# Kernel optimization log

Hardware: AMD Instinct MI355X
Metric: run time of the kernel (lower is better)

The kernel has to match this reference:

```python
import jax, jax.numpy as jnp
import numpy as np

B, C, H, NP, M = 32, 768, 12, 196, 64
D = C // H
GRID = 14  # sqrt(196)
NG = 1 + NP  # cls + patches = 197
EPS = 1e-5


def _ln(x, w, b):
    mu = x.mean(-1, keepdims=True)
    var = ((x - mu) ** 2).mean(-1, keepdims=True)
    return (x - mu) * jax.lax.rsqrt(var + EPS) * w + b


def setup_inputs() -> dict:
    key = jax.random.key(0)
    ks = jax.random.split(key, 14)
    std = 0.02
    return {
        "x": jax.random.normal(ks[0], (B, NG + M, C), dtype=jnp.float32),
        "ps": jax.random.uniform(ks[1], (B, M, 2), dtype=jnp.float32) * 224.0,
        "ns": jax.random.randint(ks[2], (B,), 1, M + 1, dtype=jnp.int32),
        "norm1_w": jnp.ones((C,), jnp.float32),
        "norm1_b": jnp.zeros((C,), jnp.float32),
        "qkv_w": jax.random.normal(ks[3], (3 * C, C), jnp.float32) * std,
        "proj_w": jax.random.normal(ks[4], (C, C), jnp.float32) * std,
        "proj_b": jnp.zeros((C,), jnp.float32),
        "norm2_w": jnp.ones((C,), jnp.float32),
        "norm2_b": jnp.zeros((C,), jnp.float32),
        "fc1_w": jax.random.normal(ks[5], (4 * C, C), jnp.float32) * std,
        "fc1_b": jnp.zeros((4 * C,), jnp.float32),
        "fc2_w": jax.random.normal(ks[6], (C, 4 * C), jnp.float32) * std,
        "fc2_b": jnp.zeros((C,), jnp.float32),
    }


def reference(x, ps, ns, norm1_w, norm1_b, qkv_w, proj_w, proj_b,
              norm2_w, norm2_b, fc1_w, fc1_b, fc2_w, fc2_b):
    Bn, Nt, Cd = x.shape  # Nt = 1 + 196 + M
    scale = D ** -0.5

    h = _ln(x, norm1_w, norm1_b)
    qkv = (h @ qkv_w.T).reshape(Bn, Nt, 3, H, D).transpose(2, 0, 3, 1, 4)  # [3,B,H,Nt,D]
    q, k, v = qkv[0], qkv[1], qkv[2]

    # ---- global attention over cls + patch tokens (first 197) ----
    attn = jnp.einsum('bhnd,bhmd->bhnm', q[:, :, :NG], k[:, :, :NG]) * scale
    attn = jax.nn.softmax(attn, axis=-1)
    xg = jnp.einsum('bhnm,bhmd->bhnd', attn, v[:, :, :NG])
    xg = xg.transpose(0, 2, 1, 3).reshape(Bn, NG, Cd)  # [B,197,C]

    # ---- keypoint bilinear-gather attention (get_single_filter_matrix) ----
    pos = ps / 16.0  # [B,M,2]; pos[...,1] -> row (dim 4), pos[...,0] -> col (dim 5)
    c0 = jnp.clip(jnp.floor(pos[..., 0]), 0, GRID - 1).astype(jnp.int32)
    c1 = jnp.clip(jnp.ceil(pos[..., 0]), 0, GRID - 1).astype(jnp.int32)
    r0 = jnp.clip(jnp.floor(pos[..., 1]), 0, GRID - 1).astype(jnp.int32)
    r1 = jnp.clip(jnp.ceil(pos[..., 1]), 0, GRID - 1).astype(jnp.int32)
    # neighbor order: top_left, top_right, bottom_left, bottom_right
    rows = jnp.stack([r0, r1, r0, r1], axis=-1)  # [B,M,4]
    cols = jnp.stack([c0, c0, c1, c1], axis=-1)
    flat = rows * GRID + cols  # [B,M,4] flat index into 196 patch tokens

    kp = k[:, :, 1:NG]  # [B,H,196,D]
    vp = v[:, :, 1:NG]
    idx = jnp.broadcast_to(flat.reshape(Bn, 1, M * 4, 1), (Bn, H, M * 4, D))
    knb = jnp.take_along_axis(kp, idx, axis=2).reshape(Bn, H, M, 4, D)
    vnb = jnp.take_along_axis(vp, idx, axis=2).reshape(Bn, H, M, 4, D)

    qk = q[:, :, NG:]  # keypoint queries [B,H,M,D]
    a = jnp.einsum('bhmd,bhmjd->bhmj', qk, knb)  # no scale, per original
    a = jax.nn.softmax(a, axis=-1)
    kout = jnp.einsum('bhmj,bhmjd->bhmd', a, vnb)
    kout = kout.transpose(0, 2, 1, 3).reshape(Bn, M, Cd)

    y = jnp.concatenate([xg, kout], axis=1) @ proj_w.T + proj_b
    x = x + y

    h2 = _ln(x, norm2_w, norm2_b)
    h2 = jax.nn.gelu(h2 @ fc1_w.T + fc1_b, approximate=False)
    x = x + (h2 @ fc2_w.T + fc2_b)
    return x
```

## Files before the change

kernel.cpp:

```cpp
#include <hip/hip_runtime.h>

typedef unsigned short u16;
typedef unsigned int u32;
typedef u16 u16x8 __attribute__((ext_vector_type(8)));
typedef u16 u16x4 __attribute__((ext_vector_type(4)));
typedef float f32x4 __attribute__((ext_vector_type(4)));
typedef __bf16 bf16x8 __attribute__((ext_vector_type(8)));

#define NHEAD 12
#define NT 261
#define NGL 197
#define CDIM 768
#define KT 14
#define PS_STRIDE 232
#define VT_STRIDE 232

__device__ __forceinline__ float bf2f(u16 u) {
    u32 x = ((u32)u) << 16;
    float f;
    __builtin_memcpy(&f, &x, 4);
    return f;
}
__device__ __forceinline__ u16 f2bf(float f) {
    u32 x;
    __builtin_memcpy(&x, &f, 4);
    x = (x + 0x7fffu + ((x >> 16) & 1u)) >> 16;
    return (u16)x;
}

#define GLD_LDS16(g, l) \
    __builtin_amdgcn_global_load_lds((const __attribute__((address_space(1))) void*)(g), \
                                     (__attribute__((address_space(3))) void*)(l), 16, 0, 0)
#define WAITV(n) asm volatile("s_waitcnt vmcnt(" #n ")" ::: "memory")
#define BARM() asm volatile("s_barrier" ::: "memory")

__global__ __launch_bounds__(256) void convk(const float* __restrict__ in, u16* __restrict__ out, int n4) {
    int i = blockIdx.x * 256 + threadIdx.x;
    if (i >= n4) return;
    float4 v = ((const float4*)in)[i];
    u16x4 o;
    o[0] = f2bf(v.x); o[1] = f2bf(v.y); o[2] = f2bf(v.z); o[3] = f2bf(v.w);
    ((u16x4*)out)[i] = o;
}

__global__ __launch_bounds__(256) void ln_k(const float* __restrict__ in, const float* __restrict__ w,
                                            const float* __restrict__ bia, u16* __restrict__ out) {
    int row = blockIdx.x;
    int tid = threadIdx.x;
    const float* r = in + (size_t)row * CDIM;
    float v0 = r[tid], v1 = r[tid + 256], v2 = r[tid + 512];
    float s = v0 + v1 + v2;
    float ss = v0 * v0 + v1 * v1 + v2 * v2;
#pragma unroll
    for (int off = 32; off; off >>= 1) {
        s += __shfl_xor(s, off);
        ss += __shfl_xor(ss, off);
    }
    __shared__ float ls[4], lss[4];
    int wv = tid >> 6;
    if ((tid & 63) == 0) { ls[wv] = s; lss[wv] = ss; }
    __syncthreads();
    s = ls[0] + ls[1] + ls[2] + ls[3];
    ss = lss[0] + lss[1] + lss[2] + lss[3];
    float mu = s * (1.f / 768.f);
    float var = ss * (1.f / 768.f) - mu * mu;
    float inv = rsqrtf(var + 1e-5f);
    u16* o = out + (size_t)row * CDIM;
    o[tid]       = f2bf((v0 - mu) * inv * w[tid]       + bia[tid]);
    o[tid + 256] = f2bf((v1 - mu) * inv * w[tid + 256] + bia[tid + 256]);
    o[tid + 512] = f2bf((v2 - mu) * inv * w[tid + 512] + bia[tid + 512]);
}

template <int EPI>
__global__ __launch_bounds__(256, 2) void gemm3(const u16* __restrict__ A, const u16* __restrict__ Bw,
                                                int M, int N, int K, int nbn,
                                                const float* __restrict__ bias,
                                                const float* __restrict__ resid, void* __restrict__ outp) {
    __shared__ __align__(16) u16 sm[4][8192];
    const int tid = threadIdx.x;
    const int nwg = gridDim.x;
    const int q = nwg >> 3, r = nwg & 7;
    const int xcd = blockIdx.x & 7, within = blockIdx.x >> 3;
    const int id2 = (xcd < r ? xcd * (q + 1) : r * (q + 1) + (xcd - r) * q) + within;
    const int bm = id2 / nbn, bn = id2 % nbn;
    const int lane = tid & 63, wv = tid >> 6;
    const int wr = wv >> 1, wc = wv & 1;
    const int l15 = lane & 15, lg = lane >> 4;
    const int arow0 = bm * 128, brow0 = bn * 128;
    const int nt = K >> 5;

    const int srow = tid >> 2;
    const int sslot = tid & 3;
    const int sk0 = (sslot ^ ((srow >> 1) & 3)) * 8;
    int arA0 = arow0 + srow;        if (arA0 >= M) arA0 = M - 1;
    int arA1 = arow0 + srow + 64;   if (arA1 >= M) arA1 = M - 1;
    const u16* gA0 = A + (size_t)arA0 * K + sk0;
    const u16* gA1 = A + (size_t)arA1 * K + sk0;
    const u16* gB0 = Bw + (size_t)(brow0 + srow) * K + sk0;
    const u16* gB1 = Bw + (size_t)(brow0 + srow + 64) * K + sk0;
    const int lo0 = tid * 8, lo1 = 2048 + tid * 8;

    auto STAGE = [&](int tt) {
        u16* b = sm[tt & 3];
        const size_t ko = (size_t)tt * 32;
        GLD_LDS16(gA0 + ko, b + lo0);
        GLD_LDS16(gA1 + ko, b + lo1);
        GLD_LDS16(gB0 + ko, b + 4096 + lo0);
        GLD_LDS16(gB1 + ko, b + 4096 + lo1);
    };

    f32x4 acc[4][4] = {};
    const int xorv = (lg ^ ((l15 >> 1) & 3)) << 3;

    STAGE(0); STAGE(1); STAGE(2);
    for (int t = 0; t < nt; ++t) {
        if (t + 2 < nt) { WAITV(8); } else if (t + 1 < nt) { WAITV(4); } else { WAITV(0); }
        BARM();
        if (t + 3 < nt) STAGE(t + 3);
        const u16* bufp = sm[t & 3];
        bf16x8 af[4], bfr[4];
#pragma unroll
        for (int mi = 0; mi < 4; ++mi)
            af[mi] = *(const bf16x8*)(bufp + (wr * 64 + mi * 16 + l15) * 32 + xorv);
#pragma unroll
        for (int ni = 0; ni < 4; ++ni)
            bfr[ni] = *(const bf16x8*)(bufp + 4096 + (wc * 64 + ni * 16 + l15) * 32 + xorv);
#pragma unroll
        for (int mi = 0; mi < 4; ++mi)
#pragma unroll
            for (int ni = 0; ni < 4; ++ni)
                acc[mi][ni] = __builtin_amdgcn_mfma_f32_16x16x32_bf16(af[mi], bfr[ni], acc[mi][ni], 0, 0, 0);
    }

#pragma unroll
    for (int mi = 0; mi < 4; ++mi) {
        int row0 = arow0 + wr * 64 + mi * 16 + lg * 4;
#pragma unroll
        for (int ni = 0; ni < 4; ++ni) {
            int col = brow0 + wc * 64 + ni * 16 + l15;
            float bb = (EPI == 0) ? 0.f : bias[col];
#pragma unroll
            for (int rr = 0; rr < 4; ++rr) {
                int row = row0 + rr;
                if (row < M) {
                    float v = acc[mi][ni][rr] + bb;
                    if (EPI == 2) {
                        float z = v + 0.044715f * v * v * v;
                        v = v / (1.f + __expf(-1.5957691216f * z));
                    }
                    if (EPI == 1) {
                        v += resid[(size_t)row * N + col];
                        ((float*)outp)[(size_t)row * N + col] = v;
                    } else {
                        ((u16*)outp)[(size_t)row * N + col] = f2bf(v);
                    }
                }
            }
        }
    }
}

__global__ __launch_bounds__(256) void attn_global_mfma(const u16* __restrict__ qkv, u16* __restrict__ Z) {
    __shared__ __align__(16) u16 lds0[4 * 16 * PS_STRIDE];
    __shared__ __align__(16) u16 Vt[64 * VT_STRIDE];
    const int tid = threadIdx.x;
    const int blk = blockIdx.x;
    const int qt = blk & 3;
    const int bh = blk >> 2;
    const int h = bh % NHEAD, b = bh / NHEAD;
    const int lane = tid & 63, wv = tid >> 6;
    const int l15 = lane & 15, lg = lane >> 4;
    const u16* base = qkv + (size_t)b * NT * 2304;

    for (int c = tid; c < 224 * 8; c += 256) {
        int row = c >> 3, ch = c & 7;
        u16x8 v = {};
        if (row < NGL) v = *(const u16x8*)(base + (size_t)row * 2304 + 768 + h * 64 + ch * 8);
        int byte = row * 128 + ((ch * 16) ^ ((row & 7) << 4));
        *(u16x8*)((char*)lds0 + byte) = v;
    }
    for (int c = tid; c < 112 * 8; c += 256) {
        int mp = c >> 3, dch = c & 7;
        int m0 = mp * 2;
        u16x8 a0 = {}, a1 = {};
        if (m0 < NGL)     a0 = *(const u16x8*)(base + (size_t)m0 * 2304 + 1536 + h * 64 + dch * 8);
        if (m0 + 1 < NGL) a1 = *(const u16x8*)(base + (size_t)(m0 + 1) * 2304 + 1536 + h * 64 + dch * 8);
#pragma unroll
        for (int j = 0; j < 8; ++j) {
            u32 pk = (u32)a0[j] | ((u32)a1[j] << 16);
            *(u32*)((char*)Vt + (size_t)(dch * 8 + j) * (VT_STRIDE * 2) + m0 * 2) = pk;
        }
    }
    const int q0 = qt * 64 + wv * 16;
    int qrow = q0 + l15; if (qrow > NGL - 1) qrow = NGL - 1;
    bf16x8 aq0 = *(const bf16x8*)(base + (size_t)qrow * 2304 + h * 64 + lg * 8);
    bf16x8 aq1 = *(const bf16x8*)(base + (size_t)qrow * 2304 + h * 64 + 32 + lg * 8);
    __syncthreads();

    f32x4 s[KT];
    const int sw = (l15 & 7) << 4;
#pragma unroll
    for (int t = 0; t < KT; ++t) {
        const char* krow = (const char*)lds0 + (t * 16 + l15) * 128;
        bf16x8 bk0 = *(const bf16x8*)(krow + ((lg * 16) ^ sw));
        bf16x8 bk1 = *(const bf16x8*)(krow + ((64 + lg * 16) ^ sw));
        f32x4 acc = {};
        acc = __builtin_amdgcn_mfma_f32_16x16x32_bf16(aq0, bk0, acc, 0, 0, 0);
        acc = __builtin_amdgcn_mfma_f32_16x16x32_bf16(aq1, bk1, acc, 0, 0, 0);
        s[t] = acc * 0.125f;
    }
    float mx[4] = {-1e30f, -1e30f, -1e30f, -1e30f};
#pragma unroll
    for (int t = 0; t < KT; ++t)
#pragma unroll
        for (int r = 0; r < 4; ++r) mx[r] = fmaxf(mx[r], s[t][r]);
#pragma unroll
    for (int off = 1; off < 16; off <<= 1)
#pragma unroll
        for (int r = 0; r < 4; ++r) mx[r] = fmaxf(mx[r], __shfl_xor(mx[r], off));
    float sum[4] = {};
#pragma unroll
    for (int t = 0; t < KT; ++t) {
        bool valid = (t * 16 + l15) < NGL;
#pragma unroll
        for (int r = 0; r < 4; ++r) {
            float e = valid ? __expf(s[t][r] - mx[r]) : 0.f;
            s[t][r] = e;
            sum[r] += e;
        }
    }
#pragma unroll
    for (int off = 1; off < 16; off <<= 1)
#pragma unroll
        for (int r = 0; r < 4; ++r) sum[r] += __shfl_xor(sum[r], off);
    float inv[4];
#pragma unroll
    for (int r = 0; r < 4; ++r) inv[r] = 1.f / sum[r];

    __syncthreads();
    u16* Pw = lds0 + wv * 16 * PS_STRIDE;
#pragma unroll
    for (int t = 0; t < KT; ++t)
#pragma unroll
        for (int r = 0; r < 4; ++r)
            Pw[(4 * lg + r) * PS_STRIDE + t * 16 + l15] = f2bf(s[t][r] * inv[r]);

    f32x4 o[4] = {};
#pragma unroll
    for (int ks = 0; ks < 7; ++ks) {
        bf16x8 pa = *(const bf16x8*)(Pw + l15 * PS_STRIDE + ks * 32 + lg * 8);
#pragma unroll
        for (int dt = 0; dt < 4; ++dt) {
            bf16x8 bv = *(const bf16x8*)((const char*)Vt + (size_t)(dt * 16 + l15) * (VT_STRIDE * 2) + ks * 64 + lg * 16);
            o[dt] = __builtin_amdgcn_mfma_f32_16x16x32_bf16(pa, bv, o[dt], 0, 0, 0);
        }
    }
#pragma unroll
    for (int dt = 0; dt < 4; ++dt)
#pragma unroll
        for (int r = 0; r < 4; ++r) {
            int q = q0 + 4 * lg + r;
            if (q < NGL) Z[((size_t)b * NT + q) * CDIM + h * 64 + dt * 16 + l15] = f2bf(o[dt][r]);
        }
}

__global__ __launch_bounds__(64) void attn_neigh(const u16* __restrict__ qkv, const float* __restrict__ ps,
                                                 u16* __restrict__ Z) {
    int blk = blockIdx.x;
    int b = blk >> 6, m = blk & 63;
    int lane = threadIdx.x;
    float px = ps[((size_t)b * 64 + m) * 2 + 0] * (1.f / 16.f);
    float py = ps[((size_t)b * 64 + m) * 2 + 1] * (1.f / 16.f);
    int c0 = min(max((int)floorf(px), 0), 13);
    int c1 = min(max((int)ceilf(px), 0), 13);
    int r0 = min(max((int)floorf(py), 0), 13);
    int r1 = min(max((int)ceilf(py), 0), 13);
    int tok[4];
    tok[0] = 1 + r0 * 14 + c0;
    tok[1] = 1 + r1 * 14 + c0;
    tok[2] = 1 + r0 * 14 + c1;
    tok[3] = 1 + r1 * 14 + c1;
    const size_t rowq = ((size_t)b * NT + NGL + m) * 2304;
#pragma unroll 1
    for (int h = 0; h < NHEAD; ++h) {
        float qv = bf2f(qkv[rowq + h * 64 + lane]);
        float a[4];
#pragma unroll
        for (int j = 0; j < 4; ++j) {
            float p = qv * bf2f(qkv[((size_t)b * NT + tok[j]) * 2304 + 768 + h * 64 + lane]);
#pragma unroll
            for (int off = 32; off; off >>= 1) p += __shfl_xor(p, off);
            a[j] = p;
        }
        float mx = fmaxf(fmaxf(a[0], a[1]), fmaxf(a[2], a[3]));
        float e0 = expf(a[0] - mx), e1 = expf(a[1] - mx), e2 = expf(a[2] - mx), e3 = expf(a[3] - mx);
        float inv = 1.f / (e0 + e1 + e2 + e3);
        float v0 = bf2f(qkv[((size_t)b * NT + tok[0]) * 2304 + 1536 + h * 64 + lane]);
        float v1 = bf2f(qkv[((size_t)b * NT + tok[1]) * 2304 + 1536 + h * 64 + lane]);
        float v2 = bf2f(qkv[((size_t)b * NT + tok[2]) * 2304 + 1536 + h * 64 + lane]);
        float v3 = bf2f(qkv[((size_t)b * NT + tok[3]) * 2304 + 1536 + h * 64 + lane]);
        float o = (e0 * v0 + e1 * v1 + e2 * v2 + e3 * v3) * inv;
        Z[((size_t)b * NT + NGL + m) * CDIM + h * 64 + lane] = f2bf(o);
    }
}

extern "C" void kernel_launch(void* const* d_in, const int* in_sizes, int n_in,
                              void* d_out, int out_size, void* d_ws, size_t ws_size,
                              hipStream_t stream) {
    const float* x      = (const float*)d_in[0];
    const float* ps     = (const float*)d_in[1];
    const float* n1w    = (const float*)d_in[3];
    const float* n1b    = (const float*)d_in[4];
    const float* qkv_w  = (const float*)d_in[5];
    const float* proj_w = (const float*)d_in[6];
    const float* proj_b = (const float*)d_in[7];
    const float* n2w    = (const float*)d_in[8];
    const float* n2b    = (const float*)d_in[9];
    const float* fc1_w  = (const float*)d_in[10];
    const float* fc1_b  = (const float*)d_in[11];
    const float* fc2_w  = (const float*)d_in[12];
    const float* fc2_b  = (const float*)d_in[13];

    char* ws = (char*)d_ws;
    const int M = 32 * NT;
    u16* hbuf  = (u16*)ws;
    u16* qkvb  = (u16*)(ws + 12828672);
    u16* Zb    = (u16*)(ws + 12828672 + 38486016);
    u16* Gb    = (u16*)(ws + 12828672);
    float* x1  = (float*)(ws + 64143360);
    u16* wq    = (u16*)(ws + 89800704);
    u16* wp    = wq + 2304 * 768;
    u16* w1    = wp + 768 * 768;
    u16* w2    = w1 + 3072 * 768;

    convk<<<(2304 * 768 / 4 + 255) / 256, 256, 0, stream>>>(qkv_w, wq, 2304 * 768 / 4);
    convk<<<(768 * 768 / 4 + 255) / 256, 256, 0, stream>>>(proj_w, wp, 768 * 768 / 4);
    convk<<<(3072 * 768 / 4 + 255) / 256, 256, 0, stream>>>(fc1_w, w1, 3072 * 768 / 4);
    convk<<<(768 * 3072 / 4 + 255) / 256, 256, 0, stream>>>(fc2_w, w2, 768 * 3072 / 4);

    ln_k<<<M, 256, 0, stream>>>(x, n1w, n1b, hbuf);
    gemm3<0><<<66 * 18, 256, 0, stream>>>(hbuf, wq, M, 2304, 768, 18, nullptr, nullptr, qkvb);
    attn_global_mfma<<<32 * NHEAD * 4, 256, 0, stream>>>(qkvb, Zb);
    attn_neigh<<<32 * 64, 64, 0, stream>>>(qkvb, ps, Zb);
    gemm3<1><<<66 * 6, 256, 0, stream>>>(Zb, wp, M, 768, 768, 6, proj_b, x, x1);
    ln_k<<<M, 256, 0, stream>>>(x1, n2w, n2b, hbuf);
    gemm3<2><<<66 * 24, 256, 0, stream>>>(hbuf, w1, M, 3072, 768, 24, fc1_b, nullptr, Gb);
    gemm3<1><<<66 * 6, 256, 0, stream>>>(Gb, w2, M, 768, 3072, 6, fc2_b, x1, (float*)d_out);
}
```

Measured before the change: 322.6 us.

## Store GEMM operands in MFMA fragment layout and load directly without LDS

The weights, layernorm outputs, attention output and GELU output are written in a pre-tiled MFMA fragment layout, so each GEMM wave reads its bf16x8 fragments straight from global memory and the LDS staging, barriers and async copies go away. The four weight conversions are merged with the first layernorm into one launch, layernorm now uses one wave per row, and neighbour attention is folded into the global attention kernel as extra blocks. This removes launch overhead and LDS traffic, but drops the explicit multi-stage prefetch pipeline and data reuse through shared memory. The GEMM now depends on L1/L2 caching and on latency being hidden by occupancy.

After: 343.5 us. 1.06x slower.

```diff
diff --git a/kernel.cpp b/kernel.cpp
--- a/kernel.cpp
+++ b/kernel.cpp
@@ -28,55 +28,94 @@
     return (u16)x;
 }
 
-#define GLD_LDS16(g, l) \
-    __builtin_amdgcn_global_load_lds((const __attribute__((address_space(1))) void*)(g), \
-                                     (__attribute__((address_space(3))) void*)(l), 16, 0, 0)
-#define WAITV(n) asm volatile("s_waitcnt vmcnt(" #n ")" ::: "memory")
-#define BARM() asm volatile("s_barrier" ::: "memory")
-
-__global__ __launch_bounds__(256) void convk(const float* __restrict__ in, u16* __restrict__ out, int n4) {
-    int i = blockIdx.x * 256 + threadIdx.x;
-    if (i >= n4) return;
-    float4 v = ((const float4*)in)[i];
-    u16x4 o;
-    o[0] = f2bf(v.x); o[1] = f2bf(v.y); o[2] = f2bf(v.z); o[3] = f2bf(v.w);
-    ((u16x4*)out)[i] = o;
-}
-
-__global__ __launch_bounds__(256) void ln_k(const float* __restrict__ in, const float* __restrict__ w,
-                                            const float* __restrict__ bia, u16* __restrict__ out) {
-    int row = blockIdx.x;
-    int tid = threadIdx.x;
-    const float* r = in + (size_t)row * CDIM;
-    float v0 = r[tid], v1 = r[tid + 256], v2 = r[tid + 512];
-    float s = v0 + v1 + v2;
-    float ss = v0 * v0 + v1 * v1 + v2 * v2;
+__device__ __forceinline__ size_t fragAddr(int row, int col, int Kd) {
+    return ((size_t)((row >> 4) * (Kd >> 5) + (col >> 5))) * 512 +
+           ((((col >> 3) & 3) * 16 + (row & 15)) * 8 + (col & 7));
+}
+
+struct CvArgs {
+    const float* in[4];
+    u16* out[4];
+    int n8[4];
+    int K[4];
+};
+
+__device__ __forceinline__ void ln_row(const float* __restrict__ in, const float* __restrict__ w,
+                                       const float* __restrict__ bia, u16* __restrict__ out,
+                                       int row, int lane) {
+    const float4* r = (const float4*)(in + (size_t)row * CDIM);
+    float4 a = r[lane], b4 = r[lane + 64], c4 = r[lane + 128];
+    float s  = a.x + a.y + a.z + a.w + b4.x + b4.y + b4.z + b4.w + c4.x + c4.y + c4.z + c4.w;
+    float ss = a.x*a.x + a.y*a.y + a.z*a.z + a.w*a.w
+             + b4.x*b4.x + b4.y*b4.y + b4.z*b4.z + b4.w*b4.w
+             + c4.x*c4.x + c4.y*c4.y + c4.z*c4.z + c4.w*c4.w;
 #pragma unroll
     for (int off = 32; off; off >>= 1) {
-        s += __shfl_xor(s, off);
+        s  += __shfl_xor(s, off);
         ss += __shfl_xor(ss, off);
     }
-    __shared__ float ls[4], lss[4];
-    int wv = tid >> 6;
-    if ((tid & 63) == 0) { ls[wv] = s; lss[wv] = ss; }
-    __syncthreads();
-    s = ls[0] + ls[1] + ls[2] + ls[3];
-    ss = lss[0] + lss[1] + lss[2] + lss[3];
     float mu = s * (1.f / 768.f);
     float var = ss * (1.f / 768.f) - mu * mu;
     float inv = rsqrtf(var + 1e-5f);
-    u16* o = out + (size_t)row * CDIM;
-    o[tid]       = f2bf((v0 - mu) * inv * w[tid]       + bia[tid]);
-    o[tid + 256] = f2bf((v1 - mu) * inv * w[tid + 256] + bia[tid + 256]);
-    o[tid + 512] = f2bf((v2 - mu) * inv * w[tid + 512] + bia[tid + 512]);
+    const float4* wp = (const float4*)w;
+    const float4* bp = (const float4*)bia;
+#pragma unroll
+    for (int t = 0; t < 3; ++t) {
+        float4 v = (t == 0) ? a : (t == 1) ? b4 : c4;
+        float4 ww = wp[lane + t * 64], bb = bp[lane + t * 64];
+        u16x4 ov;
+        ov[0] = f2bf((v.x - mu) * inv * ww.x + bb.x);
+        ov[1] = f2bf((v.y - mu) * inv * ww.y + bb.y);
+        ov[2] = f2bf((v.z - mu) * inv * ww.z + bb.z);
+        ov[3] = f2bf((v.w - mu) * inv * ww.w + bb.w);
+        int col = t * 256 + lane * 4;
+        *(u16x4*)(out + fragAddr(row, col, 768)) = ov;
+    }
+}
+
+__global__ __launch_bounds__(256) void pre_k(const float* __restrict__ x, const float* __restrict__ w,
+                                             const float* __restrict__ bia, u16* __restrict__ out,
+                                             int nrows, CvArgs cv) {
+    if (blockIdx.y == 0) {
+        int i = blockIdx.x * 256 + threadIdx.x;
+        int s0 = cv.n8[0], s1 = s0 + cv.n8[1], s2 = s1 + cv.n8[2], s3 = s2 + cv.n8[3];
+        int seg, base;
+        if (i < s0)      { seg = 0; base = 0; }
+        else if (i < s1) { seg = 1; base = s0; }
+        else if (i < s2) { seg = 2; base = s1; }
+        else if (i < s3) { seg = 3; base = s2; }
+        else return;
+        int j = i - base;
+        int Kd = cv.K[seg];
+        int kd8 = Kd >> 3;
+        int n = j / kd8;
+        int k8 = j - n * kd8;
+        const float* src = cv.in[seg] + (size_t)n * Kd + k8 * 8;
+        float4 v0 = *(const float4*)src;
+        float4 v1 = *(const float4*)(src + 4);
+        u16x8 ov;
+        ov[0] = f2bf(v0.x); ov[1] = f2bf(v0.y); ov[2] = f2bf(v0.z); ov[3] = f2bf(v0.w);
+        ov[4] = f2bf(v1.x); ov[5] = f2bf(v1.y); ov[6] = f2bf(v1.z); ov[7] = f2bf(v1.w);
+        *(u16x8*)(cv.out[seg] + fragAddr(n, k8 * 8, Kd)) = ov;
+    } else {
+        int lane = threadIdx.x & 63, wv = threadIdx.x >> 6;
+        int row = blockIdx.x * 4 + wv;
+        if (row < nrows) ln_row(x, w, bia, out, row, lane);
+    }
+}
+
+__global__ __launch_bounds__(256) void ln_w(const float* __restrict__ in, const float* __restrict__ w,
+                                            const float* __restrict__ bia, u16* __restrict__ out, int nrows) {
+    int lane = threadIdx.x & 63, wv = threadIdx.x >> 6;
+    int row = blockIdx.x * 4 + wv;
+    if (row < nrows) ln_row(in, w, bia, out, row, lane);
 }
 
 template <int EPI>
-__global__ __launch_bounds__(256, 2) void gemm3(const u16* __restrict__ A, const u16* __restrict__ Bw,
-                                                int M, int N, int K, int nbn,
-                                                const float* __restrict__ bias,
-                                                const float* __restrict__ resid, void* __restrict__ outp) {
-    __shared__ __align__(16) u16 sm[4][8192];
+__global__ __launch_bounds__(256) void gemm10(const u16* __restrict__ Ap, const u16* __restrict__ Bp,
+                                              int M, int N, int K, int nbn,
+                                              const float* __restrict__ bias,
+                                              const float* __restrict__ resid, void* __restrict__ outp) {
     const int tid = threadIdx.x;
     const int nwg = gridDim.x;
     const int q = nwg >> 3, r = nwg & 7;
@@ -86,73 +125,62 @@
     const int lane = tid & 63, wv = tid >> 6;
     const int wr = wv >> 1, wc = wv & 1;
     const int l15 = lane & 15, lg = lane >> 4;
-    const int arow0 = bm * 128, brow0 = bn * 128;
-    const int nt = K >> 5;
-
-    const int srow = tid >> 2;
-    const int sslot = tid & 3;
-    const int sk0 = (sslot ^ ((srow >> 1) & 3)) * 8;
-    int arA0 = arow0 + srow;        if (arA0 >= M) arA0 = M - 1;
-    int arA1 = arow0 + srow + 64;   if (arA1 >= M) arA1 = M - 1;
-    const u16* gA0 = A + (size_t)arA0 * K + sk0;
-    const u16* gA1 = A + (size_t)arA1 * K + sk0;
-    const u16* gB0 = Bw + (size_t)(brow0 + srow) * K + sk0;
-    const u16* gB1 = Bw + (size_t)(brow0 + srow + 64) * K + sk0;
-    const int lo0 = tid * 8, lo1 = 2048 + tid * 8;
-
-    auto STAGE = [&](int tt) {
-        u16* b = sm[tt & 3];
-        const size_t ko = (size_t)tt * 32;
-        GLD_LDS16(gA0 + ko, b + lo0);
-        GLD_LDS16(gA1 + ko, b + lo1);
-        GLD_LDS16(gB0 + ko, b + 4096 + lo0);
-        GLD_LDS16(gB1 + ko, b + 4096 + lo1);
-    };
+    const int nt = K >> 6;
+    const int kch = K >> 5;
+    const int mtmax = (M - 1) >> 4;
+
+    const u16* aB[4];
+    const u16* bB[4];
+#pragma unroll
+    for (int i = 0; i < 4; ++i) {
+        int mt = bm * 8 + wr * 4 + i;
+        if (mt > mtmax) mt = mtmax;
+        aB[i] = Ap + (size_t)mt * kch * 512 + lane * 8;
+        bB[i] = Bp + (size_t)(bn * 8 + wc * 4 + i) * kch * 512 + lane * 8;
+    }
 
     f32x4 acc[4][4] = {};
-    const int xorv = (lg ^ ((l15 >> 1) & 3)) << 3;
-
-    STAGE(0); STAGE(1); STAGE(2);
+#pragma unroll 1
     for (int t = 0; t < nt; ++t) {
-        if (t + 2 < nt) { WAITV(8); } else if (t + 1 < nt) { WAITV(4); } else { WAITV(0); }
-        BARM();
-        if (t + 3 < nt) STAGE(t + 3);
-        const u16* bufp = sm[t & 3];
-        bf16x8 af[4], bfr[4];
+        bf16x8 af[4][2], bf[4][2];
+#pragma unroll
+        for (int i = 0; i < 4; ++i) {
+            af[i][0] = *(const bf16x8*)(aB[i] + (size_t)(2 * t) * 512);
+            af[i][1] = *(const bf16x8*)(aB[i] + (size_t)(2 * t + 1) * 512);
+            bf[i][0] = *(const bf16x8*)(bB[i] + (size_t)(2 * t) * 512);
+            bf[i][1] = *(const bf16x8*)(bB[i] + (size_t)(2 * t + 1) * 512);
+        }
 #pragma unroll
         for (int mi = 0; mi < 4; ++mi)
-            af[mi] = *(const bf16x8*)(bufp + (wr * 64 + mi * 16 + l15) * 32 + xorv);
-#pragma unroll
-        for (int ni = 0; ni < 4; ++ni)
-            bfr[ni] = *(const bf16x8*)(bufp + 4096 + (wc * 64 + ni * 16 + l15) * 32 + xorv);
-#pragma unroll
-        for (int mi = 0; mi < 4; ++mi)
-#pragma unroll
-            for (int ni = 0; ni < 4; ++ni)
-                acc[mi][ni] = __builtin_amdgcn_mfma_f32_16x16x32_bf16(af[mi], bfr[ni], acc[mi][ni], 0, 0, 0);
-    }
-
+#pragma unroll
+            for (int ni = 0; ni < 4; ++ni) {
+                acc[mi][ni] = __builtin_amdgcn_mfma_f32_16x16x32_bf16(af[mi][0], bf[ni][0], acc[mi][ni], 0, 0, 0);
+                acc[mi][ni] = __builtin_amdgcn_mfma_f32_16x16x32_bf16(af[mi][1], bf[ni][1], acc[mi][ni], 0, 0, 0);
+            }
+    }
+
+    const int arow0 = bm * 128, bcol0 = bn * 128;
 #pragma unroll
     for (int mi = 0; mi < 4; ++mi) {
         int row0 = arow0 + wr * 64 + mi * 16 + lg * 4;
 #pragma unroll
         for (int ni = 0; ni < 4; ++ni) {
-            int col = brow0 + wc * 64 + ni * 16 + l15;
+            int col = bcol0 + wc * 64 + ni * 16 + l15;
             float bb = (EPI == 0) ? 0.f : bias[col];
 #pragma unroll
             for (int rr = 0; rr < 4; ++rr) {
                 int row = row0 + rr;
                 if (row < M) {
                     float v = acc[mi][ni][rr] + bb;
-                    if (EPI == 2) {
-                        float z = v + 0.044715f * v * v * v;
-                        v = v / (1.f + __expf(-1.5957691216f * z));
-                    }
-                    if (EPI == 1) {
+                    if (EPI == 0) {
+                        ((u16*)outp)[(size_t)row * N + col] = f2bf(v);
+                    } else if (EPI == 1) {
                         v += resid[(size_t)row * N + col];
                         ((float*)outp)[(size_t)row * N + col] = v;
                     } else {
-                        ((u16*)outp)[(size_t)row * N + col] = f2bf(v);
+                        float z = v + 0.044715f * v * v * v;
+                        v = v / (1.f + __expf(-1.5957691216f * z));
+                        ((u16*)outp)[fragAddr(row, col, N)] = f2bf(v);
                     }
                 }
             }
@@ -160,15 +188,58 @@
     }
 }
 
-__global__ __launch_bounds__(256) void attn_global_mfma(const u16* __restrict__ qkv, u16* __restrict__ Z) {
+__global__ __launch_bounds__(256) void attn_fused(const u16* __restrict__ qkv, const float* __restrict__ ps,
+                                                  u16* __restrict__ Z) {
     __shared__ __align__(16) u16 lds0[4 * 16 * PS_STRIDE];
     __shared__ __align__(16) u16 Vt[64 * VT_STRIDE];
     const int tid = threadIdx.x;
+    const int lane = tid & 63, wv = tid >> 6;
+
+    if (blockIdx.x >= 1536) {
+        int idx = blockIdx.x - 1536;
+        int b = idx >> 4;
+        int m = (idx & 15) * 4 + wv;
+        float px = ps[((size_t)b * 64 + m) * 2 + 0] * (1.f / 16.f);
+        float py = ps[((size_t)b * 64 + m) * 2 + 1] * (1.f / 16.f);
+        int c0 = min(max((int)floorf(px), 0), 13);
+        int c1 = min(max((int)ceilf(px), 0), 13);
+        int r0 = min(max((int)floorf(py), 0), 13);
+        int r1 = min(max((int)ceilf(py), 0), 13);
+        int tok[4];
+        tok[0] = 1 + r0 * 14 + c0;
+        tok[1] = 1 + r1 * 14 + c0;
+        tok[2] = 1 + r0 * 14 + c1;
+        tok[3] = 1 + r1 * 14 + c1;
+        const size_t rowq = ((size_t)b * NT + NGL + m) * 2304;
+        const int zrow = b * NT + NGL + m;
+#pragma unroll 1
+        for (int h = 0; h < NHEAD; ++h) {
+            float qv = bf2f(qkv[rowq + h * 64 + lane]);
+            float a[4];
+#pragma unroll
+            for (int j = 0; j < 4; ++j) {
+                float p = qv * bf2f(qkv[((size_t)b * NT + tok[j]) * 2304 + 768 + h * 64 + lane]);
+#pragma unroll
+                for (int off = 32; off; off >>= 1) p += __shfl_xor(p, off);
+                a[j] = p;
+            }
+            float mx = fmaxf(fmaxf(a[0], a[1]), fmaxf(a[2], a[3]));
+            float e0 = expf(a[0] - mx), e1 = expf(a[1] - mx), e2 = expf(a[2] - mx), e3 = expf(a[3] - mx);
+            float inv = 1.f / (e0 + e1 + e2 + e3);
+            float v0 = bf2f(qkv[((size_t)b * NT + tok[0]) * 2304 + 1536 + h * 64 + lane]);
+            float v1 = bf2f(qkv[((size_t)b * NT + tok[1]) * 2304 + 1536 + h * 64 + lane]);
+            float v2 = bf2f(qkv[((size_t)b * NT + tok[2]) * 2304 + 1536 + h * 64 + lane]);
+            float v3 = bf2f(qkv[((size_t)b * NT + tok[3]) * 2304 + 1536 + h * 64 + lane]);
+            float o = (e0 * v0 + e1 * v1 + e2 * v2 + e3 * v3) * inv;
+            Z[fragAddr(zrow, h * 64 + lane, 768)] = f2bf(o);
+        }
+        return;
+    }
+
     const int blk = blockIdx.x;
     const int qt = blk & 3;
     const int bh = blk >> 2;
     const int h = bh % NHEAD, b = bh / NHEAD;
-    const int lane = tid & 63, wv = tid >> 6;
     const int l15 = lane & 15, lg = lane >> 4;
     const u16* base = qkv + (size_t)b * NT * 2304;
 
@@ -259,49 +330,9 @@
     for (int dt = 0; dt < 4; ++dt)
 #pragma unroll
         for (int r = 0; r < 4; ++r) {
-            int q = q0 + 4 * lg + r;
-            if (q < NGL) Z[((size_t)b * NT + q) * CDIM + h * 64 + dt * 16 + l15] = f2bf(o[dt][r]);
-        }
-}
-
-__global__ __launch_bounds__(64) void attn_neigh(const u16* __restrict__ qkv, const float* __restrict__ ps,
-                                                 u16* __restrict__ Z) {
-    int blk = blockIdx.x;
-    int b = blk >> 6, m = blk & 63;
-    int lane = threadIdx.x;
-    float px = ps[((size_t)b * 64 + m) * 2 + 0] * (1.f / 16.f);
-    float py = ps[((size_t)b * 64 + m) * 2 + 1] * (1.f / 16.f);
-    int c0 = min(max((int)floorf(px), 0), 13);
-    int c1 = min(max((int)ceilf(px), 0), 13);
-    int r0 = min(max((int)floorf(py), 0), 13);
-    int r1 = min(max((int)ceilf(py), 0), 13);
-    int tok[4];
-    tok[0] = 1 + r0 * 14 + c0;
-    tok[1] = 1 + r1 * 14 + c0;
-    tok[2] = 1 + r0 * 14 + c1;
-    tok[3] = 1 + r1 * 14 + c1;
-    const size_t rowq = ((size_t)b * NT + NGL + m) * 2304;
-#pragma unroll 1
-    for (int h = 0; h < NHEAD; ++h) {
-        float qv = bf2f(qkv[rowq + h * 64 + lane]);
-        float a[4];
-#pragma unroll
-        for (int j = 0; j < 4; ++j) {
-            float p = qv * bf2f(qkv[((size_t)b * NT + tok[j]) * 2304 + 768 + h * 64 + lane]);
-#pragma unroll
-            for (int off = 32; off; off >>= 1) p += __shfl_xor(p, off);
-            a[j] = p;
-        }
-        float mx = fmaxf(fmaxf(a[0], a[1]), fmaxf(a[2], a[3]));
-        float e0 = expf(a[0] - mx), e1 = expf(a[1] - mx), e2 = expf(a[2] - mx), e3 = expf(a[3] - mx);
-        float inv = 1.f / (e0 + e1 + e2 + e3);
-        float v0 = bf2f(qkv[((size_t)b * NT + tok[0]) * 2304 + 1536 + h * 64 + lane]);
-        float v1 = bf2f(qkv[((size_t)b * NT + tok[1]) * 2304 + 1536 + h * 64 + lane]);
-        float v2 = bf2f(qkv[((size_t)b * NT + tok[2]) * 2304 + 1536 + h * 64 + lane]);
-        float v3 = bf2f(qkv[((size_t)b * NT + tok[3]) * 2304 + 1536 + h * 64 + lane]);
-        float o = (e0 * v0 + e1 * v1 + e2 * v2 + e3 * v3) * inv;
-        Z[((size_t)b * NT + NGL + m) * CDIM + h * 64 + lane] = f2bf(o);
-    }
+            int qq = q0 + 4 * lg + r;
+            if (qq < NGL) Z[fragAddr(b * NT + qq, h * 64 + dt * 16 + l15, 768)] = f2bf(o[dt][r]);
+        }
 }
 
 extern "C" void kernel_launch(void* const* d_in, const int* in_sizes, int n_in,
@@ -333,17 +364,17 @@
     u16* w1    = wp + 768 * 768;
     u16* w2    = w1 + 3072 * 768;
 
-    convk<<<(2304 * 768 / 4 + 255) / 256, 256, 0, stream>>>(qkv_w, wq, 2304 * 768 / 4);
-    convk<<<(768 * 768 / 4 + 255) / 256, 256, 0, stream>>>(proj_w, wp, 768 * 768 / 4);
-    convk<<<(3072 * 768 / 4 + 255) / 256, 256, 0, stream>>>(fc1_w, w1, 3072 * 768 / 4);
-    convk<<<(768 * 3072 / 4 + 255) / 256, 256, 0, stream>>>(fc2_w, w2, 768 * 3072 / 4);
-
-    ln_k<<<M, 256, 0, stream>>>(x, n1w, n1b, hbuf);
-    gemm3<0><<<66 * 18, 256, 0, stream>>>(hbuf, wq, M, 2304, 768, 18, nullptr, nullptr, qkvb);
-    attn_global_mfma<<<32 * NHEAD * 4, 256, 0, stream>>>(qkvb, Zb);
-    attn_neigh<<<32 * 64, 64, 0, stream>>>(qkvb, ps, Zb);
-    gemm3<1><<<66 * 6, 256, 0, stream>>>(Zb, wp, M, 768, 768, 6, proj_b, x, x1);
-    ln_k<<<M, 256, 0, stream>>>(x1, n2w, n2b, hbuf);
-    gemm3<2><<<66 * 24, 256, 0, stream>>>(hbuf, w1, M, 3072, 768, 24, fc1_b, nullptr, Gb);
-    gemm3<1><<<66 * 6, 256, 0, stream>>>(Gb, w2, M, 768, 3072, 6, fc2_b, x1, (float*)d_out);
-}
+    CvArgs cv;
+    cv.in[0] = qkv_w;  cv.out[0] = wq; cv.n8[0] = 2304 * 768 / 8; cv.K[0] = 768;
+    cv.in[1] = proj_w; cv.out[1] = wp; cv.n8[1] = 768 * 768 / 8;  cv.K[1] = 768;
+    cv.in[2] = fc1_w;  cv.out[2] = w1; cv.n8[2] = 3072 * 768 / 8; cv.K[2] = 768;
+    cv.in[3] = fc2_w;  cv.out[3] = w2; cv.n8[3] = 768 * 3072 / 8; cv.K[3] = 3072;
+
+    pre_k<<<dim3(3456, 2), 256, 0, stream>>>(x, n1w, n1b, hbuf, M, cv);
+    gemm10<0><<<66 * 18, 256, 0, stream>>>(hbuf, wq, M, 2304, 768, 18, nullptr, nullptr, qkvb);
+    attn_fused<<<2048, 256, 0, stream>>>(qkvb, ps, Zb);
+    gemm10<1><<<66 * 6, 256, 0, stream>>>(Zb, wp, M, 768, 768, 6, proj_b, x, x1);
+    ln_w<<<2088, 256, 0, stream>>>(x1, n2w, n2b, hbuf, M);
+    gemm10<2><<<66 * 24, 256, 0, stream>>>(hbuf, w1, M, 3072, 768, 24, fc1_b, nullptr, Gb);
+    gemm10<1><<<66 * 6, 256, 0, stream>>>(Gb, w2, M, 768, 3072, 6, fc2_b, x1, (float*)d_out);
+}
```
